# Performance work log

Measured on AMD Instinct MI355X. Metric: run time of the kernel, lower is better.

## Reference

```python
import jax, jax.numpy as jnp
import numpy as np

NUM_HEADS = 8  # init num_heads


def setup_inputs() -> dict:
    key = jax.random.key(0)
    ks = jax.random.split(key, 8)
    B, N, C, G = 2, 256 * 256, 256, 512  # N hardcoded by original reshape(256*256)
    xq = jax.random.normal(ks[0], (B, N, C), jnp.float32)
    xk = jax.random.normal(ks[1], (B, N, C), jnp.float32)
    xv = jax.random.normal(ks[2], (B, N, C), jnp.float32)
    w_scale = C ** -0.5
    Wq = jax.random.normal(ks[3], (C, C), jnp.float32) * w_scale
    bq = jax.random.normal(ks[4], (C,), jnp.float32) * 0.02
    Wp = jax.random.normal(ks[5], (C, C), jnp.float32) * w_scale
    bp = jax.random.normal(ks[6], (C,), jnp.float32) * 0.02
    # Voronoi cell labels 1..G, each cell exactly N//G tokens, randomly scattered
    # over the 256x256 grid (irregular gather/scatter access, all cells < 1500 tokens).
    labels = jnp.repeat(jnp.arange(1, G + 1, dtype=jnp.int32), N // G)
    Voronoi = jnp.stack([
        jax.random.permutation(jax.random.fold_in(ks[7], b), labels) for b in range(B)
    ]).reshape(B, 256, 256)
    return {"xq": xq, "xk": xk, "xv": xv, "Wq": Wq, "bq": bq,
            "Wp": Wp, "bp": bp, "Voronoi": Voronoi, "num_groups": G}


def reference(xq, xk, xv, Wq, bq, Wp, bp, Voronoi, num_groups):
    B, N, C = xq.shape
    H = NUM_HEADS
    hd = C // H
    scale = hd ** -0.5  # qk_scale default: head_dim ** -0.5
    # NOTE: the original forward projects q, k AND v with self.q (shared weights/bias).
    # This (likely a bug upstream) is preserved faithfully here.
    q = (xq @ Wq.T + bq).reshape(B, N, H, hd)
    k = (xk @ Wq.T + bq).reshape(B, N, H, hd)
    v = (xv @ Wq.T + bq).reshape(B, N, H, hd)
    labels = Voronoi.reshape(B, N)
    order = jnp.argsort(labels, axis=1)   # [B, N] sort tokens by Voronoi cell id
    inv = jnp.argsort(order, axis=1)      # inverse permutation for scatter-back
    S = N // num_groups                   # tokens per cell (static)

    def gather(t):  # [B, N, H, hd] -> [B, G, S, H, hd] grouped by cell
        return jnp.take_along_axis(t, order[:, :, None, None], axis=1).reshape(B, num_groups, S, H, hd)

    qg = gather(q) * scale
    kg = gather(k)
    vg = gather(v)
    attn = jnp.einsum('bgshd,bgthd->bghst', qg, kg)   # per-cell scores [B,G,H,S,S]
    p = jax.nn.softmax(attn, axis=-1)                 # attn_drop=0 (eval)
    og = jnp.einsum('bghst,bgthd->bgshd', p, vg).reshape(B, N, H, hd)
    out = jnp.take_along_axis(og, inv[:, :, None, None], axis=1).reshape(B, N, C)
    return out @ Wp.T + bp                            # proj_drop=0 (eval)
```

## Files before the change

### kernel.cpp

```cpp
#include <hip/hip_runtime.h>
#include <hip/hip_bf16.h>

#define B_    2
#define NTOK  65536
#define C_    256
#define H_    8
#define HD_   32
#define G_    512
#define S_    128
#define BN    (B_*NTOK)
#define M3    (3*BN)

typedef __attribute__((ext_vector_type(8))) short short8;
typedef __attribute__((ext_vector_type(4))) float f32x4;

__device__ __forceinline__ ushort f2bf(float f) {
  __bf16 h = (__bf16)f;
  return __builtin_bit_cast(unsigned short, h);
}
__device__ __forceinline__ unsigned pk2(float lo, float hi) {
  return (unsigned)f2bf(lo) | ((unsigned)f2bf(hi) << 16);
}

__device__ __forceinline__ void gl16(const void* g, void* l) {
  __builtin_amdgcn_global_load_lds(
      (const __attribute__((address_space(1))) unsigned int*)g,
      (__attribute__((address_space(3))) unsigned int*)l, 16, 0, 0);
}

#define SW4(c, r) ((((c) ^ (r) ^ ((r) >> 2))) & 3)
#define SWK32(c, r) ((((c) ^ ((r) >> 1))) & 3)

__global__ __launch_bounds__(256) void k_prep(const float* __restrict__ Wq,
                                              const float* __restrict__ Wp,
                                              ushort* __restrict__ Wq_img,
                                              ushort* __restrict__ Wp_img) {
  int gid = blockIdx.x * 256 + threadIdx.x;
  int w = gid >> 13, rem = gid & 8191;
  if (w == 0) {
    int ks = rem >> 11, rem2 = rem & 2047;
    int r = rem2 >> 3, c = rem2 & 7;
    const float4* s = reinterpret_cast<const float4*>(Wq + (size_t)r * 256 + ks * 64 + c * 8);
    float4 a = s[0], b = s[1];
    uint4 o;
    o.x = pk2(a.x, a.y); o.y = pk2(a.z, a.w);
    o.z = pk2(b.x, b.y); o.w = pk2(b.z, b.w);
    *reinterpret_cast<uint4*>(Wq_img + ks * 16384 + r * 64 + ((c ^ (r & 7)) << 3)) = o;
  } else {
    int h = rem >> 10, r = (rem >> 2) & 255, c = rem & 3;
    const float4* s = reinterpret_cast<const float4*>(Wp + (size_t)r * 256 + h * 32 + c * 8);
    float4 a = s[0], b = s[1];
    uint4 o;
    o.x = pk2(a.x, a.y); o.y = pk2(a.z, a.w);
    o.z = pk2(b.x, b.y); o.w = pk2(b.z, b.w);
    *reinterpret_cast<uint4*>(Wp_img + h * 8192 + r * 32 + (SWK32(c, r) << 3)) = o;
  }
}

__global__ __launch_bounds__(256) void k_group(const int* __restrict__ vor,
                                               int* __restrict__ grp,
                                               int* __restrict__ cnt) {
  int idx = blockIdx.x * 256 + threadIdx.x;
  int b = idx >> 16;
  int n = idx & (NTOK - 1);
  int g = vor[idx] - 1;
  int pos = atomicAdd(&cnt[(b << 9) + g], 1);
  grp[((b << 9) + g) * S_ + pos] = n;
}

__global__ __launch_bounds__(512, 4) void k_proj_qkv(
    const float* __restrict__ xq, const float* __restrict__ xk,
    const float* __restrict__ xv, const ushort* __restrict__ Wq_img,
    const float* __restrict__ bq, ushort* __restrict__ qkv) {
  __shared__ ushort As[128 * 64];
  __shared__ ushort Bs[2][256 * 64];
  int mt = blockIdx.x;
  int t = mt >> 10;
  const float* A = (t == 0) ? xq : (t == 1) ? xk : xv;
  size_t abase = (size_t)(mt & 1023) * 128 * 256;
  int row0 = mt * 128;

  int tid = threadIdx.x, lane = tid & 63, wave = tid >> 6;
  int l15 = lane & 15, hi = lane >> 4;
  int wr = (wave >> 2) * 64, wc = (wave & 3) * 64;
  int sr = tid >> 2, sq = tid & 3;

  const float* aptr = A + abase + (size_t)sr * 256 + sq * 16;
  int boff = wave * 4096 + lane * 16;

  f32x4 acc[4][4] = {};
  float4 ar[2][4];
  {
    const float4* p = reinterpret_cast<const float4*>(aptr);
#pragma unroll
    for (int j = 0; j < 4; ++j) ar[0][j] = p[j];
  }
#pragma unroll
  for (int j = 0; j < 4; ++j)
    gl16((const char*)Wq_img + boff + j * 1024, (char*)Bs[0] + boff + j * 1024);

#pragma unroll
  for (int ks = 0; ks < 4; ++ks) {
    uint4 w0, w1;
    w0.x = pk2(ar[ks & 1][0].x, ar[ks & 1][0].y); w0.y = pk2(ar[ks & 1][0].z, ar[ks & 1][0].w);
    w0.z = pk2(ar[ks & 1][1].x, ar[ks & 1][1].y); w0.w = pk2(ar[ks & 1][1].z, ar[ks & 1][1].w);
    w1.x = pk2(ar[ks & 1][2].x, ar[ks & 1][2].y); w1.y = pk2(ar[ks & 1][2].z, ar[ks & 1][2].w);
    w1.z = pk2(ar[ks & 1][3].x, ar[ks & 1][3].y); w1.w = pk2(ar[ks & 1][3].z, ar[ks & 1][3].w);
    *reinterpret_cast<uint4*>(&As[sr * 64 + (((sq * 2) ^ (sr & 7)) << 3)]) = w0;
    *reinterpret_cast<uint4*>(&As[sr * 64 + (((sq * 2 + 1) ^ (sr & 7)) << 3)]) = w1;
    if (ks < 3) {
      const float4* p = reinterpret_cast<const float4*>(aptr + (ks + 1) * 64);
#pragma unroll
      for (int j = 0; j < 4; ++j) ar[(ks + 1) & 1][j] = p[j];
#pragma unroll
      for (int j = 0; j < 4; ++j)
        gl16((const char*)Wq_img + (ks + 1) * 32768 + boff + j * 1024,
             (char*)Bs[(ks + 1) & 1] + boff + j * 1024);
      asm volatile("s_waitcnt vmcnt(8)" ::: "memory");
    } else {
      asm volatile("s_waitcnt vmcnt(0)" ::: "memory");
    }
    asm volatile("s_waitcnt lgkmcnt(0)" ::: "memory");
    __builtin_amdgcn_s_barrier();
    const ushort* Bcur = Bs[ks & 1];
#pragma unroll
    for (int kk = 0; kk < 2; ++kk) {
      int ck = kk * 4 + hi;
      short8 af[4], bfr[4];
#pragma unroll
      for (int m = 0; m < 4; ++m) {
        int r = wr + m * 16 + l15;
        af[m] = *reinterpret_cast<const short8*>(&As[r * 64 + ((ck ^ (r & 7)) << 3)]);
      }
#pragma unroll
      for (int n = 0; n < 4; ++n) {
        int r = wc + n * 16 + l15;
        bfr[n] = *reinterpret_cast<const short8*>(&Bcur[r * 64 + ((ck ^ (r & 7)) << 3)]);
      }
#pragma unroll
      for (int m = 0; m < 4; ++m)
#pragma unroll
        for (int n = 0; n < 4; ++n)
          acc[m][n] = __builtin_amdgcn_mfma_f32_16x16x32_bf16(af[m], bfr[n], acc[m][n], 0, 0, 0);
    }
    asm volatile("s_waitcnt lgkmcnt(0)" ::: "memory");
    __builtin_amdgcn_s_barrier();
  }

  ushort* Ot = (ushort*)Bs;
#pragma unroll
  for (int n = 0; n < 4; ++n) {
    int col = wc + n * 16 + l15;
    float bv = bq[col];
    int c = col >> 3, ci = col & 7;
#pragma unroll
    for (int m = 0; m < 4; ++m) {
      int r0 = wr + m * 16 + hi * 4;
#pragma unroll
      for (int j = 0; j < 4; ++j) {
        int r = r0 + j;
        int slot = c ^ (((r >> 2) & 3) << 1);
        Ot[r * 256 + slot * 8 + ci] = f2bf(acc[m][n][j] + bv);
      }
    }
  }
  __syncthreads();
  {
    size_t gbase = (size_t)row0 * 256;
#pragma unroll
    for (int s = 0; s < 8; ++s) {
      int off = s * 4096 + tid * 8;
      int r = off >> 8, cc = (off >> 3) & 31;
      int slot = cc ^ (((r >> 2) & 3) << 1);
      *reinterpret_cast<uint4*>(qkv + gbase + off) =
          *reinterpret_cast<const uint4*>(Ot + r * 256 + slot * 8);
    }
  }
}

__global__ __launch_bounds__(512) void k_attn_proj(
    const ushort* __restrict__ qkv, const int* __restrict__ grp,
    const ushort* __restrict__ Wp_img, const float* __restrict__ bp,
    float* __restrict__ out) {
  __shared__ int toks[128];
  __shared__ ushort PsB[128 * 128];
  __shared__ ushort Vt[32 * 128];
  __shared__ ushort Oh[128 * 32];
  __shared__ ushort WpS[256 * 32];
  ushort* Qs = PsB;
  ushort* Ks = PsB + 4096;
  ushort* Ps = PsB;

  int bid = blockIdx.x;
  int g = bid & (G_ - 1), b = bid >> 9;
  int tid = threadIdx.x, lane = tid & 63, wave = tid >> 6;
  int l15 = lane & 15, hi = lane >> 4;
  int strip = wave * 16;
  int mg = wave >> 1, ng = wave & 1;

  if (tid < 128) toks[tid] = grp[((b << 9) + g) * S_ + tid];
  __syncthreads();

  int wpoff = wave * 1024 + lane * 16;
  gl16((const char*)Wp_img + wpoff, (char*)WpS + wpoff);
  gl16((const char*)Wp_img + 8192 + wpoff, (char*)WpS + wpoff + 8192);

  f32x4 acc[2][8] = {};

  int r_st = tid >> 2, cp = tid & 3;
  int tok_st = toks[r_st];
  size_t rowq = (size_t)(b * NTOK + tok_st) * 256;

  for (int h = 0; h < 8; ++h) {
    {
      size_t base = rowq + h * 32 + cp * 8;
      uint4 qa = *reinterpret_cast<const uint4*>(qkv + base);
      uint4 ka = *reinterpret_cast<const uint4*>(qkv + (size_t)BN * 256 + base);
      uint4 va = *reinterpret_cast<const uint4*>(qkv + (size_t)2 * BN * 256 + base);
      *reinterpret_cast<uint4*>(&Qs[r_st * 32 + SW4(cp, r_st) * 8]) = qa;
      *reinterpret_cast<uint4*>(&Ks[r_st * 32 + SW4(cp, r_st) * 8]) = ka;
      int chunk_t = r_st >> 3, tl = r_st & 7;
      const ushort* pv_ = reinterpret_cast<const ushort*>(&va);
#pragma unroll
      for (int e = 0; e < 8; ++e) {
        int ch = cp * 8 + e;
        Vt[ch * 128 + ((chunk_t ^ ((ch & 7) << 1)) << 3) + tl] = pv_[e];
      }
    }
    asm volatile("s_waitcnt lgkmcnt(0)" ::: "memory");
    __builtin_amdgcn_s_barrier();

    f32x4 sacc[8] = {};
    {
      int ra = strip + l15;
      short8 aq = *reinterpret_cast<const short8*>(&Qs[ra * 32 + SW4(hi, ra) * 8]);
      short8 bk[8];
#pragma unroll
      for (int n = 0; n < 8; ++n) {
        int r = n * 16 + l15;
        bk[n] = *reinterpret_cast<const short8*>(&Ks[r * 32 + SW4(hi, r) * 8]);
      }
#pragma unroll
      for (int n = 0; n < 8; ++n)
        sacc[n] = __builtin_amdgcn_mfma_f32_16x16x32_bf16(aq, bk[n], sacc[n], 0, 0, 0);
    }
    asm volatile("s_waitcnt lgkmcnt(0)" ::: "memory");
    __builtin_amdgcn_s_barrier();

    const float cexp = 0.17677669529663687f * 1.4426950408889634f;
#pragma unroll
    for (int j = 0; j < 4; ++j) {
      float mx = -1e30f;
#pragma unroll
      for (int n = 0; n < 8; ++n) mx = fmaxf(mx, sacc[n][j]);
#pragma unroll
      for (int d = 1; d < 16; d <<= 1) mx = fmaxf(mx, __shfl_xor(mx, d));
      float pv[8], sum = 0.f;
#pragma unroll
      for (int n = 0; n < 8; ++n) { pv[n] = exp2f((sacc[n][j] - mx) * cexp); sum += pv[n]; }
#pragma unroll
      for (int d = 1; d < 16; d <<= 1) sum += __shfl_xor(sum, d);
      float inv = 1.0f / sum;
      int row = strip + hi * 4 + j;
#pragma unroll
      for (int n = 0; n < 8; ++n) {
        int col = n * 16 + l15;
        int chunk = col >> 3;
        Ps[row * 128 + ((chunk ^ (row & 7)) << 3) + (col & 7)] = f2bf(pv[n] * inv);
      }
    }
    asm volatile("s_waitcnt lgkmcnt(0)" ::: "memory");
    __builtin_amdgcn_s_barrier();

    f32x4 oacc[2] = {};
#pragma unroll
    for (int kk = 0; kk < 4; ++kk) {
      int chunk = kk * 4 + hi;
      int rp = strip + l15;
      short8 pa = *reinterpret_cast<const short8*>(&Ps[rp * 128 + ((chunk ^ (rp & 7)) << 3)]);
      short8 bv[2];
#pragma unroll
      for (int n = 0; n < 2; ++n) {
        int ch = n * 16 + l15;
        bv[n] = *reinterpret_cast<const short8*>(&Vt[ch * 128 + ((chunk ^ ((ch & 7) << 1)) << 3)]);
      }
#pragma unroll
      for (int n = 0; n < 2; ++n)
        oacc[n] = __builtin_amdgcn_mfma_f32_16x16x32_bf16(pa, bv[n], oacc[n], 0, 0, 0);
    }
#pragma unroll
    for (int n = 0; n < 2; ++n) {
#pragma unroll
      for (int j = 0; j < 4; ++j) {
        int row = strip + hi * 4 + j;
        int col = n * 16 + l15;
        Oh[row * 32 + (SWK32(col >> 3, row) << 3) + (col & 7)] = f2bf(oacc[n][j]);
      }
    }
    asm volatile("s_waitcnt vmcnt(0)" ::: "memory");
    asm volatile("s_waitcnt lgkmcnt(0)" ::: "memory");
    __builtin_amdgcn_s_barrier();

    {
      short8 af[2], bf[8];
#pragma unroll
      for (int m = 0; m < 2; ++m) {
        int r = mg * 32 + m * 16 + l15;
        af[m] = *reinterpret_cast<const short8*>(&Oh[r * 32 + (SWK32(hi, r) << 3)]);
      }
#pragma unroll
      for (int n = 0; n < 8; ++n) {
        int r = ng * 128 + n * 16 + l15;
        bf[n] = *reinterpret_cast<const short8*>(&WpS[r * 32 + (SWK32(hi, r) << 3)]);
      }
#pragma unroll
      for (int m = 0; m < 2; ++m)
#pragma unroll
        for (int n = 0; n < 8; ++n)
          acc[m][n] = __builtin_amdgcn_mfma_f32_16x16x32_bf16(af[m], bf[n], acc[m][n], 0, 0, 0);
    }
    asm volatile("s_waitcnt lgkmcnt(0)" ::: "memory");
    __builtin_amdgcn_s_barrier();
    if (h < 7) {
      gl16((const char*)Wp_img + (h + 1) * 16384 + wpoff, (char*)WpS + wpoff);
      gl16((const char*)Wp_img + (h + 1) * 16384 + 8192 + wpoff, (char*)WpS + wpoff + 8192);
    }
  }

  float* Of = (float*)PsB;
#pragma unroll
  for (int q = 0; q < 4; ++q) {
    __syncthreads();
    if (mg == q) {
#pragma unroll
      for (int n = 0; n < 8; ++n) {
        int col = ng * 128 + n * 16 + l15;
        float bv = bp[col];
        int c = col >> 2, ci = col & 3;
#pragma unroll
        for (int m = 0; m < 2; ++m) {
#pragma unroll
          for (int j = 0; j < 4; ++j) {
            int lr = m * 16 + hi * 4 + j;
            int slot = c ^ (((lr >> 2) & 3) << 2);
            Of[lr * 256 + slot * 4 + ci] = acc[m][n][j] + bv;
          }
        }
      }
    }
    __syncthreads();
#pragma unroll
    for (int s = 0; s < 4; ++s) {
      int off = s * 2048 + tid * 4;
      int lr = off >> 8, cc = (off >> 2) & 63;
      int slot = cc ^ (((lr >> 2) & 3) << 2);
      int tok = toks[q * 32 + lr];
      *reinterpret_cast<float4*>(out + ((size_t)(b * NTOK + tok)) * 256 + cc * 4) =
          *reinterpret_cast<const float4*>(Of + lr * 256 + slot * 4);
    }
  }
}

extern "C" void kernel_launch(void* const* d_in, const int* in_sizes, int n_in,
                              void* d_out, int out_size, void* d_ws, size_t ws_size,
                              hipStream_t stream) {
  const float* xq = (const float*)d_in[0];
  const float* xk = (const float*)d_in[1];
  const float* xv = (const float*)d_in[2];
  const float* Wq = (const float*)d_in[3];
  const float* bq = (const float*)d_in[4];
  const float* Wp = (const float*)d_in[5];
  const float* bp = (const float*)d_in[6];
  const int*   vor = (const int*)d_in[7];

  char* ws = (char*)d_ws;
  ushort* qkv    = (ushort*)ws;
  int*    grp    = (int*)(ws + (size_t)201326592);
  int*    cnt    = (int*)(ws + (size_t)201850880);
  ushort* Wq_img = (ushort*)(ws + (size_t)201854976);
  ushort* Wp_img = (ushort*)(ws + (size_t)201986048);

  hipMemsetAsync(cnt, 0, B_ * G_ * sizeof(int), stream);
  k_prep<<<dim3(64), dim3(256), 0, stream>>>(Wq, Wp, Wq_img, Wp_img);
  k_group<<<dim3(BN / 256), dim3(256), 0, stream>>>(vor, grp, cnt);
  k_proj_qkv<<<dim3(M3 / 128), dim3(512), 0, stream>>>(xq, xk, xv, Wq_img, bq, qkv);
  k_attn_proj<<<dim3(B_ * G_), dim3(512), 0, stream>>>(qkv, grp, Wp_img, bp, (float*)d_out);
}
```

Baseline: 341.7 us.

## Prefetch next head QKV, fold softmax scale into Q, defer normalization

The attention kernel now loads the next head's Q/K/V rows from global memory into registers right after the LDS barrier, so the gather latency overlaps the current head's compute. The softmax scale times log2(e) is folded into the Q projection epilogue, which removes a multiply per exponent. Normalization by the row sum moves to the output, and one barrier between the P write and the PV read is dropped because each wave reads only its own strip. New XOR swizzles for the P and V^T tiles aim to cut LDS bank conflicts; the unnormalized bf16 P values slightly change rounding.

```diff
diff --git a/kernel.cpp b/kernel.cpp
--- a/kernel.cpp
+++ b/kernel.cpp
@@ -30,6 +30,10 @@
 
 #define SW4(c, r) ((((c) ^ (r) ^ ((r) >> 2))) & 3)
 #define SWK32(c, r) ((((c) ^ ((r) >> 1))) & 3)
+#define PSL(c, r) ((((c) ^ ((r) & 7) ^ ((((r) >> 3) & 1) << 1))) & 15)
+#define VSL(c, ch) ((((c) ^ (((ch) & 7) << 1) ^ (((ch) >> 3) & 3))) & 15)
+
+#define QSCALE 0.25506907131737264f
 
 __global__ __launch_bounds__(256) void k_prep(const float* __restrict__ Wq,
                                               const float* __restrict__ Wp,
@@ -77,6 +81,7 @@
   int mt = blockIdx.x;
   int t = mt >> 10;
   const float* A = (t == 0) ? xq : (t == 1) ? xk : xv;
+  float qsc = (t == 0) ? QSCALE : 1.0f;
   size_t abase = (size_t)(mt & 1023) * 128 * 256;
   int row0 = mt * 128;
 
@@ -160,7 +165,7 @@
       for (int j = 0; j < 4; ++j) {
         int r = r0 + j;
         int slot = c ^ (((r >> 2) & 3) << 1);
-        Ot[r * 256 + slot * 8 + ci] = f2bf(acc[m][n][j] + bv);
+        Ot[r * 256 + slot * 8 + ci] = f2bf((acc[m][n][j] + bv) * qsc);
       }
     }
   }
@@ -210,25 +215,36 @@
   int r_st = tid >> 2, cp = tid & 3;
   int tok_st = toks[r_st];
   size_t rowq = (size_t)(b * NTOK + tok_st) * 256;
+  int chunk_t = r_st >> 3, tl = r_st & 7;
+
+  uint4 qa, ka, va;
+  {
+    size_t base = rowq + cp * 8;
+    qa = *reinterpret_cast<const uint4*>(qkv + base);
+    ka = *reinterpret_cast<const uint4*>(qkv + (size_t)BN * 256 + base);
+    va = *reinterpret_cast<const uint4*>(qkv + (size_t)2 * BN * 256 + base);
+  }
 
   for (int h = 0; h < 8; ++h) {
+    *reinterpret_cast<uint4*>(&Qs[r_st * 32 + SW4(cp, r_st) * 8]) = qa;
+    *reinterpret_cast<uint4*>(&Ks[r_st * 32 + SW4(cp, r_st) * 8]) = ka;
     {
-      size_t base = rowq + h * 32 + cp * 8;
-      uint4 qa = *reinterpret_cast<const uint4*>(qkv + base);
-      uint4 ka = *reinterpret_cast<const uint4*>(qkv + (size_t)BN * 256 + base);
-      uint4 va = *reinterpret_cast<const uint4*>(qkv + (size_t)2 * BN * 256 + base);
-      *reinterpret_cast<uint4*>(&Qs[r_st * 32 + SW4(cp, r_st) * 8]) = qa;
-      *reinterpret_cast<uint4*>(&Ks[r_st * 32 + SW4(cp, r_st) * 8]) = ka;
-      int chunk_t = r_st >> 3, tl = r_st & 7;
       const ushort* pv_ = reinterpret_cast<const ushort*>(&va);
 #pragma unroll
       for (int e = 0; e < 8; ++e) {
         int ch = cp * 8 + e;
-        Vt[ch * 128 + ((chunk_t ^ ((ch & 7) << 1)) << 3) + tl] = pv_[e];
-      }
-    }
-    asm volatile("s_waitcnt lgkmcnt(0)" ::: "memory");
-    __builtin_amdgcn_s_barrier();
+        Vt[ch * 128 + (VSL(chunk_t, ch) << 3) + tl] = pv_[e];
+      }
+    }
+    asm volatile("s_waitcnt lgkmcnt(0)" ::: "memory");
+    __builtin_amdgcn_s_barrier();
+
+    if (h < 7) {
+      size_t base = rowq + (h + 1) * 32 + cp * 8;
+      qa = *reinterpret_cast<const uint4*>(qkv + base);
+      ka = *reinterpret_cast<const uint4*>(qkv + (size_t)BN * 256 + base);
+      va = *reinterpret_cast<const uint4*>(qkv + (size_t)2 * BN * 256 + base);
+    }
 
     f32x4 sacc[8] = {};
     {
@@ -247,7 +263,7 @@
     asm volatile("s_waitcnt lgkmcnt(0)" ::: "memory");
     __builtin_amdgcn_s_barrier();
 
-    const float cexp = 0.17677669529663687f * 1.4426950408889634f;
+    float inv[4];
 #pragma unroll
     for (int j = 0; j < 4; ++j) {
       float mx = -1e30f;
@@ -257,32 +273,31 @@
       for (int d = 1; d < 16; d <<= 1) mx = fmaxf(mx, __shfl_xor(mx, d));
       float pv[8], sum = 0.f;
 #pragma unroll
-      for (int n = 0; n < 8; ++n) { pv[n] = exp2f((sacc[n][j] - mx) * cexp); sum += pv[n]; }
+      for (int n = 0; n < 8; ++n) { pv[n] = exp2f(sacc[n][j] - mx); sum += pv[n]; }
 #pragma unroll
       for (int d = 1; d < 16; d <<= 1) sum += __shfl_xor(sum, d);
-      float inv = 1.0f / sum;
+      inv[j] = 1.0f / sum;
       int row = strip + hi * 4 + j;
 #pragma unroll
       for (int n = 0; n < 8; ++n) {
         int col = n * 16 + l15;
         int chunk = col >> 3;
-        Ps[row * 128 + ((chunk ^ (row & 7)) << 3) + (col & 7)] = f2bf(pv[n] * inv);
-      }
-    }
-    asm volatile("s_waitcnt lgkmcnt(0)" ::: "memory");
-    __builtin_amdgcn_s_barrier();
+        Ps[row * 128 + (PSL(chunk, row) << 3) + (col & 7)] = f2bf(pv[n]);
+      }
+    }
+    asm volatile("s_waitcnt lgkmcnt(0)" ::: "memory");
 
     f32x4 oacc[2] = {};
 #pragma unroll
     for (int kk = 0; kk < 4; ++kk) {
       int chunk = kk * 4 + hi;
       int rp = strip + l15;
-      short8 pa = *reinterpret_cast<const short8*>(&Ps[rp * 128 + ((chunk ^ (rp & 7)) << 3)]);
+      short8 pa = *reinterpret_cast<const short8*>(&Ps[rp * 128 + (PSL(chunk, rp) << 3)]);
       short8 bv[2];
 #pragma unroll
       for (int n = 0; n < 2; ++n) {
         int ch = n * 16 + l15;
-        bv[n] = *reinterpret_cast<const short8*>(&Vt[ch * 128 + ((chunk ^ ((ch & 7) << 1)) << 3)]);
+        bv[n] = *reinterpret_cast<const short8*>(&Vt[ch * 128 + (VSL(chunk, ch) << 3)]);
       }
 #pragma unroll
       for (int n = 0; n < 2; ++n)
@@ -294,7 +309,7 @@
       for (int j = 0; j < 4; ++j) {
         int row = strip + hi * 4 + j;
         int col = n * 16 + l15;
-        Oh[row * 32 + (SWK32(col >> 3, row) << 3) + (col & 7)] = f2bf(oacc[n][j]);
+        Oh[row * 32 + (SWK32(col >> 3, row) << 3) + (col & 7)] = f2bf(oacc[n][j] * inv[j]);
       }
     }
     asm volatile("s_waitcnt vmcnt(0)" ::: "memory");
```

New measurement: 325.3 us. 4.8% less time.
